# Kernel tuning notes

Measured on AMD Instinct MI355X. Metric: run time of the kernel, lower is better.

## Reference

```python
import jax, jax.numpy as jnp
import numpy as np

B, S, H = 1024, 128, 1024   # batch, seq_len, bert hidden size
E, HID, K, C = 16, 1024, 4, 3  # experts, expert hidden, top_k, num_classes
EPS = 1e-5


def _ln(x, g, b):
    mu = x.mean(-1, keepdims=True)
    var = ((x - mu) ** 2).mean(-1, keepdims=True)
    return (x - mu) / jnp.sqrt(var + EPS) * g + b


def setup_inputs() -> dict:
    key = jax.random.key(0)
    ks = jax.random.split(key, 24)
    n = lambda k, shape, s=0.02: jax.random.normal(k, shape, jnp.float32) * s
    return {
        "hidden_states": jax.random.normal(ks[0], (B, S, H), jnp.float32),
        # original BertClassificationHead
        "Wd": n(ks[1], (H, H)), "bd": jnp.zeros((H,), jnp.float32),
        "Wo": n(ks[2], (H, C)), "bo": jnp.zeros((C,), jnp.float32),
        # router
        "Wr": n(ks[3], (H, E)), "br": jnp.zeros((E,), jnp.float32),
        # stacked experts: Linear(H,HID) -> LN -> GELU -> Linear(HID,HID)
        "We1": n(ks[4], (E, H, HID)), "be1": jnp.zeros((E, HID), jnp.float32),
        "g1": jnp.ones((E, HID), jnp.float32), "beta1": jnp.zeros((E, HID), jnp.float32),
        "We2": n(ks[5], (E, HID, HID)), "be2": jnp.zeros((E, HID), jnp.float32),
        # expert_output_proj
        "Wp": n(ks[6], (HID, C)), "bp": jnp.zeros((C,), jnp.float32),
        # final_classifier: Linear(2C, C) -> LN -> ReLU -> Linear(C, C)
        "Wf1": n(ks[7], (2 * C, C)), "bf1": jnp.zeros((C,), jnp.float32),
        "gf": jnp.ones((C,), jnp.float32), "betaf": jnp.zeros((C,), jnp.float32),
        "Wf2": n(ks[8], (C, C)), "bf2": jnp.zeros((C,), jnp.float32),
    }


def reference(hidden_states, Wd, bd, Wo, bo, Wr, br, We1, be1, g1, beta1,
              We2, be2, Wp, bp, Wf1, bf1, gf, betaf, Wf2, bf2):
    cls = hidden_states[:, 0]                                   # [B,H]
    # original classifier head (dropout = identity in eval)
    original_logits = jnp.tanh(cls @ Wd + bd) @ Wo + bo         # [B,C]
    # router: top-k softmax scattered into dense [B,E] weights
    router_logits = cls @ Wr + br                               # [B,E]
    topk_vals, topk_idx = jax.lax.top_k(router_logits, K)
    topk_probs = jax.nn.softmax(topk_vals, axis=-1)
    routing_weights = jnp.zeros_like(router_logits).at[
        jnp.arange(cls.shape[0])[:, None], topk_idx].set(topk_probs)
    # experts consume mean-pooled sequence (MLPExpert mean over dim=1)
    m = hidden_states.mean(axis=1)                              # [B,H]
    h = jnp.einsum('bh,ehd->bed', m, We1) + be1                 # [B,E,HID]
    h = jax.nn.gelu(_ln(h, g1, beta1), approximate=False)
    h = jnp.einsum('bed,edf->bef', h, We2) + be2                # [B,E,HID]
    expert_logits = h @ Wp + bp                                 # [B,E,C]
    # weighted combine; routing_weights is zero for non-selected experts,
    # so this equals the sparse top-k dispatch of the original loop
    moe_output = jnp.einsum('be,bec->bc', routing_weights, expert_logits)
    combined = jnp.concatenate([original_logits, moe_output], axis=1)  # [B,2C]
    z = _ln(combined @ Wf1 + bf1, gf, betaf)
    return jax.nn.relu(z) @ Wf2 + bf2                           # [B,C]
```

## Files before the change

kernel.cpp:

```cpp
#include <hip/hip_runtime.h>
#include <math.h>

#define B_ 1024
#define S_ 128
#define H_ 1024
#define E_ 16
#define HID_ 1024
#define K_ 4
#define C_ 3
#define EPS_ 1e-5f

#define NB_CLSG 128
#define OFF_MEAN (NB_CLSG)
#define NB_MEAN 512
#define OFF_WC (OFF_MEAN + NB_MEAN)
#define NB_WC 2048
#define OFF_RT (OFF_WC + NB_WC)
#define NB_RT 128
#define OFF_BC (OFF_RT + NB_RT)
#define NB_BC 2
#define NB_P1 (OFF_BC + NB_BC)

typedef __attribute__((ext_vector_type(8))) __bf16 bf16x8;
typedef __attribute__((ext_vector_type(4))) float f32x4;
typedef __attribute__((ext_vector_type(4))) float fvec4;
typedef __attribute__((ext_vector_type(4))) unsigned short usvec4;
typedef __attribute__((ext_vector_type(8))) unsigned short usvec8;

__device__ __forceinline__ ushort bf16_rn(float f) {
  unsigned u = __float_as_uint(f);
  u += 0x7FFF + ((u >> 16) & 1);
  return (ushort)(u >> 16);
}
__device__ __forceinline__ float bf16_to_f(ushort h) {
  return __uint_as_float(((unsigned)h) << 16);
}
__device__ __forceinline__ void split2(float f, ushort& h, ushort& l) {
  h = bf16_rn(f);
  l = bf16_rn(f - bf16_to_f(h));
}
__device__ __forceinline__ void gload_lds16(const void* g, void* l) {
  __builtin_amdgcn_global_load_lds((const __attribute__((address_space(1))) void*)g,
                                   (__attribute__((address_space(3))) void*)l, 16, 0, 0);
}
#define DMA_DRAIN() do {                                  \
    asm volatile("s_waitcnt vmcnt(0)" ::: "memory");      \
    __builtin_amdgcn_sched_barrier(0);                    \
  } while (0)

__device__ __forceinline__ fvec4 nt_load4f(const float* p) {
  return __builtin_nontemporal_load((const fvec4*)p);
}
__device__ __forceinline__ void st4us(ushort* p, ushort a, ushort b, ushort c, ushort d) {
  usvec4 v; v.x = a; v.y = b; v.z = c; v.w = d;
  *(usvec4*)p = v;
}
__device__ __forceinline__ void nt_store1f(float* p, float v) {
  __builtin_nontemporal_store(v, p);
}
__device__ __forceinline__ void waveRed3(float& s0, float& s1, float& s2) {
#pragma unroll
  for (int off = 32; off; off >>= 1) {
    s0 += __shfl_down(s0, off); s1 += __shfl_down(s1, off); s2 += __shfl_down(s2, off);
  }
}

__global__ __launch_bounds__(512) void phase1_kernel(
    const float* __restrict__ hs,
    const float* __restrict__ Wd,
    const float* __restrict__ We2, const float* __restrict__ Wp, const float* __restrict__ bp,
    const float* __restrict__ Wr, const float* __restrict__ br,
    const float* __restrict__ be2,
    ushort* __restrict__ m_hi, ushort* __restrict__ m_lo,
    float* __restrict__ Wcomb, float* __restrict__ bcomb,
    int* __restrict__ topk_idx, float* __restrict__ topk_prob,
    int* __restrict__ counts, int* __restrict__ pairlist,
    float* __restrict__ tA, float* __restrict__ tB) {
  __shared__ __align__(16) ushort ldsAh0[4096], ldsAl0[4096], ldsBh0[4096], ldsBl0[4096];
  __shared__ __align__(16) ushort ldsAh1[4096], ldsAl1[4096], ldsBh1[4096], ldsBl1[4096];
  const int blk = blockIdx.x;
  const int tid = threadIdx.x;
  const int w = tid >> 6, lane = tid & 63;

  if (blk < NB_CLSG) {
    const int n0 = (blk & 7) * 128;
    const int yy = blk >> 3;
    const int mt = yy >> 1, kh = yy & 1;
    const int m0 = mt * 128;
    const int kbase = kh * 512;
    const float* sbase[2];
    size_t kstride;
    int subs0;
    if (w < 4) {
      kstride = 1;
      subs0 = w * 2;
#pragma unroll
      for (int sl = 0; sl < 2; ++sl) {
        int s = subs0 + sl;
        int b = m0 + s * 16 + (lane & 15);
        sbase[sl] = hs + (size_t)b * (S_ * H_) + ((lane >> 4) << 3);
      }
    } else {
      kstride = H_;
      subs0 = (w - 4) * 2;
#pragma unroll
      for (int sl = 0; sl < 2; ++sl) {
        int s = subs0 + sl;
        int col = n0 + s * 16 + (lane & 15);
        sbase[sl] = Wd + col + (size_t)((lane >> 4) << 3) * H_;
      }
    }
    const int wr = w >> 2, wc = w & 3;
    f32x4 acc[4][2] = {};

    auto stage = [&](int kofs, ushort* dAh, ushort* dAl, ushort* dBh, ushort* dBl) {
      ushort* dh = (w < 4) ? dAh : dBh;
      ushort* dl = (w < 4) ? dAl : dBl;
#pragma unroll
      for (int sl = 0; sl < 2; ++sl) {
        const float* p = sbase[sl] + (size_t)kofs * kstride;
        float f[8];
        if (w < 4) {
          fvec4 v0 = nt_load4f(p);
          fvec4 v1 = nt_load4f(p + 4);
          f[0] = v0.x; f[1] = v0.y; f[2] = v0.z; f[3] = v0.w;
          f[4] = v1.x; f[5] = v1.y; f[6] = v1.z; f[7] = v1.w;
        } else {
#pragma unroll
          for (int j = 0; j < 8; ++j) f[j] = p[(size_t)j * H_];
        }
        usvec8 vh, vl;
#pragma unroll
        for (int j = 0; j < 8; ++j) {
          ushort hi, lo;
          split2(f[j], hi, lo);
          vh[j] = hi; vl[j] = lo;
        }
        const int off = (subs0 + sl) * 512 + lane * 8;
        *(usvec8*)&dh[off] = vh;
        *(usvec8*)&dl[off] = vl;
      }
    };
    auto compute = [&](const ushort* Ah, const ushort* Al,
                       const ushort* Bh, const ushort* Bl) {
      bf16x8 ah[4], al[4], bh[2], bl[2];
#pragma unroll
      for (int i = 0; i < 4; ++i) {
        int off = (wr * 4 + i) * 512 + lane * 8;
        ah[i] = *(const bf16x8*)&Ah[off];
        al[i] = *(const bf16x8*)&Al[off];
      }
#pragma unroll
      for (int j = 0; j < 2; ++j) {
        int off = (wc * 2 + j) * 512 + lane * 8;
        bh[j] = *(const bf16x8*)&Bh[off];
        bl[j] = *(const bf16x8*)&Bl[off];
      }
#pragma unroll
      for (int i = 0; i < 4; ++i)
#pragma unroll
        for (int j = 0; j < 2; ++j) {
          acc[i][j] = __builtin_amdgcn_mfma_f32_16x16x32_bf16(ah[i], bh[j], acc[i][j], 0, 0, 0);
          acc[i][j] = __builtin_amdgcn_mfma_f32_16x16x32_bf16(ah[i], bl[j], acc[i][j], 0, 0, 0);
          acc[i][j] = __builtin_amdgcn_mfma_f32_16x16x32_bf16(al[i], bh[j], acc[i][j], 0, 0, 0);
        }
    };

    stage(kbase, ldsAh0, ldsAl0, ldsBh0, ldsBl0);
    DMA_DRAIN();
    __syncthreads();
#pragma unroll 1
    for (int tt = 0; tt < 8; ++tt) {
      const int t0 = tt * 2;
      stage(kbase + (t0 + 1) * 32, ldsAh1, ldsAl1, ldsBh1, ldsBl1);
      compute(ldsAh0, ldsAl0, ldsBh0, ldsBl0);
      DMA_DRAIN();
      __syncthreads();
      if (tt < 7) stage(kbase + (t0 + 2) * 32, ldsAh0, ldsAl0, ldsBh0, ldsBl0);
      compute(ldsAh1, ldsAl1, ldsBh1, ldsBl1);
      DMA_DRAIN();
      __syncthreads();
    }
    const int lr = (lane >> 4) << 2, lc = lane & 15;
    float* tp = kh ? tB : tA;
#pragma unroll
    for (int i = 0; i < 4; ++i) {
      int row = m0 + wr * 64 + i * 16 + lr;
#pragma unroll
      for (int j = 0; j < 2; ++j) {
        int col = n0 + wc * 32 + j * 16 + lc;
#pragma unroll
        for (int r = 0; r < 4; ++r)
          nt_store1f(&tp[(size_t)(row + r) * H_ + col], acc[i][j][r]);
      }
    }
  } else if (blk < OFF_WC) {
    int gid = (blk - OFF_MEAN) * 512 + tid;
    int b = gid >> 8;
    int h4 = (gid & 255) << 2;
    const float* p = hs + (size_t)b * S_ * H_ + h4;
    fvec4 v0 = nt_load4f(p);
    float sx = v0.x, sy = v0.y, sz = v0.z, sw = v0.w;
#pragma unroll 8
    for (int s = 1; s < S_; ++s) {
      fvec4 v = nt_load4f(p + (size_t)s * H_);
      sx += v.x; sy += v.y; sz += v.z; sw += v.w;
    }
    const float inv = 1.0f / (float)S_;
    float mv[4] = {sx * inv, sy * inv, sz * inv, sw * inv};
    ushort mh[4], ml[4];
#pragma unroll
    for (int i = 0; i < 4; ++i) split2(mv[i], mh[i], ml[i]);
    size_t o = (size_t)b * H_ + h4;
    st4us(&m_hi[o], mh[0], mh[1], mh[2], mh[3]);
    st4us(&m_lo[o], ml[0], ml[1], ml[2], ml[3]);
  } else if (blk < OFF_RT) {
    const int row = (blk - OFF_WC) * 8 + w;
    const float* wrp = We2 + (size_t)row * HID_;
    float s0 = 0, s1 = 0, s2 = 0;
#pragma unroll
    for (int it = 0; it < 4; ++it) {
      const int f0 = it * 256 + lane * 4;
      fvec4 v = nt_load4f(&wrp[f0]);
      s0 = fmaf(v.x, Wp[(f0 + 0) * 3 + 0], s0);
      s1 = fmaf(v.x, Wp[(f0 + 0) * 3 + 1], s1);
      s2 = fmaf(v.x, Wp[(f0 + 0) * 3 + 2], s2);
      s0 = fmaf(v.y, Wp[(f0 + 1) * 3 + 0], s0);
      s1 = fmaf(v.y, Wp[(f0 + 1) * 3 + 1], s1);
      s2 = fmaf(v.y, Wp[(f0 + 1) * 3 + 2], s2);
      s0 = fmaf(v.z, Wp[(f0 + 2) * 3 + 0], s0);
      s1 = fmaf(v.z, Wp[(f0 + 2) * 3 + 1], s1);
      s2 = fmaf(v.z, Wp[(f0 + 2) * 3 + 2], s2);
      s0 = fmaf(v.w, Wp[(f0 + 3) * 3 + 0], s0);
      s1 = fmaf(v.w, Wp[(f0 + 3) * 3 + 1], s1);
      s2 = fmaf(v.w, Wp[(f0 + 3) * 3 + 2], s2);
    }
    waveRed3(s0, s1, s2);
    if (lane == 0) {
      Wcomb[row * 3 + 0] = s0; Wcomb[row * 3 + 1] = s1; Wcomb[row * 3 + 2] = s2;
    }
  } else if (blk < OFF_BC) {
    const int b = (blk - OFF_RT) * 8 + w;
    const float* cls = hs + (size_t)b * S_ * H_;
    const int e = lane & 15, part = lane >> 4;
    float sum = 0.0f;
    for (int i = part * 256; i < part * 256 + 256; ++i)
      sum = fmaf(cls[i], Wr[i * E_ + e], sum);
    sum += __shfl_down(sum, 32);
    sum += __shfl_down(sum, 16);
    float lg[E_];
#pragma unroll
    for (int i = 0; i < E_; ++i) lg[i] = __shfl(sum, i);
    if (lane == 0) {
      for (int i = 0; i < E_; ++i) lg[i] += br[i];
      int idx[K_]; float tv[K_];
      for (int k = 0; k < K_; ++k) {
        int bi = 0; float bv = -1e30f;
        for (int i = 0; i < E_; ++i) { if (lg[i] > bv) { bv = lg[i]; bi = i; } }
        idx[k] = bi; tv[k] = bv; lg[bi] = -1e30f;
      }
      float mx = tv[0], ssum = 0.0f, p[K_];
      for (int k = 0; k < K_; ++k) { p[k] = expf(tv[k] - mx); ssum += p[k]; }
      for (int k = 0; k < K_; ++k) {
        p[k] /= ssum;
        topk_idx[b * K_ + k] = idx[k];
        topk_prob[b * K_ + k] = p[k];
        int pos = atomicAdd(&counts[idx[k]], 1);
        pairlist[idx[k] * B_ + pos] = b * K_ + k;
      }
    }
  } else {
    const int e = (blk - OFF_BC) * 8 + w;
    const float* wrp = be2 + (size_t)e * HID_;
    float s0 = 0, s1 = 0, s2 = 0;
    for (int f = lane; f < HID_; f += 64) {
      float v = wrp[f];
      s0 = fmaf(v, Wp[f * 3 + 0], s0);
      s1 = fmaf(v, Wp[f * 3 + 1], s1);
      s2 = fmaf(v, Wp[f * 3 + 2], s2);
    }
    waveRed3(s0, s1, s2);
    if (lane == 0) {
      bcomb[e * 3 + 0] = s0 + bp[0]; bcomb[e * 3 + 1] = s1 + bp[1]; bcomb[e * 3 + 2] = s2 + bp[2];
    }
  }
}

__global__ __launch_bounds__(512) void expert_gemm(
    const ushort* __restrict__ m_hi, const ushort* __restrict__ m_lo,
    const float* __restrict__ We1,
    const int* __restrict__ counts, const int* __restrict__ pairlist,
    float* __restrict__ h1A, float* __restrict__ h1B) {
  __shared__ __align__(16) ushort ldsAh0[4096], ldsAl0[4096], ldsBh0[4096], ldsBl0[4096];
  __shared__ __align__(16) ushort ldsAh1[4096], ldsAl1[4096], ldsBh1[4096], ldsBl1[4096];
  const int z = blockIdx.z;
  const int tid = threadIdx.x;
  const int lane = tid & 63, w = tid >> 6;
  const int mt = blockIdx.y >> 1, kh = blockIdx.y & 1;
  const int m0 = mt * 128, n0 = blockIdx.x * 128;
  const int kbase = kh * 512;
  const int n_e = counts[z];
  if (m0 >= n_e) return;

  const ushort* srcp[4];
  ushort* dstA0 = nullptr; ushort* dstA1 = nullptr;
  const float* bbase[2];
  int bsub[2];
  const int halfq = w & 1;
  if (w < 4) {
    const int warr = w >> 1;
    dstA0 = (warr == 0) ? ldsAh0 : ldsAl0;
    dstA1 = (warr == 0) ? ldsAh1 : ldsAl1;
    const ushort* sbase = (warr == 0) ? m_hi : m_lo;
#pragma unroll
    for (int sl = 0; sl < 4; ++sl) {
      int s = halfq * 4 + sl;
      int r = m0 + s * 16 + (lane & 15);
      if (r >= n_e) r = n_e - 1;
      r = pairlist[z * B_ + r] >> 2;
      srcp[sl] = sbase + (size_t)r * H_ + ((lane >> 4) << 3);
    }
  } else {
    const float* Wfp = We1 + (size_t)z * H_ * HID_;
#pragma unroll
    for (int sl = 0; sl < 2; ++sl) {
      int s = (w - 4) * 2 + sl;
      bsub[sl] = s;
      int col = n0 + s * 16 + (lane & 15);
      bbase[sl] = Wfp + col + (size_t)((lane >> 4) << 3) * HID_;
    }
  }

  const int wr = w >> 2, wc = w & 3;
  f32x4 acc[4][2] = {};

  auto stageA = [&](int kofs, ushort* dst) {
#pragma unroll
    for (int sl = 0; sl < 4; ++sl)
      gload_lds16(srcp[sl] + kofs, dst + (halfq * 4 + sl) * 512);
  };
  auto stageB = [&](int kofs, ushort* dBh, ushort* dBl) {
#pragma unroll
    for (int sl = 0; sl < 2; ++sl) {
      const float* bp = bbase[sl] + (size_t)kofs * HID_;
      float f[8];
#pragma unroll
      for (int j = 0; j < 8; ++j) f[j] = bp[(size_t)j * HID_];
      usvec8 vh, vl;
#pragma unroll
      for (int j = 0; j < 8; ++j) {
        ushort hi, lo;
        split2(f[j], hi, lo);
        vh[j] = hi; vl[j] = lo;
      }
      const int off = bsub[sl] * 512 + lane * 8;
      *(usvec8*)&dBh[off] = vh;
      *(usvec8*)&dBl[off] = vl;
    }
  };
  auto stage_buf0 = [&](int kofs) {
    if (w < 4) stageA(kofs, dstA0);
    else stageB(kofs, ldsBh0, ldsBl0);
  };
  auto stage_buf1 = [&](int kofs) {
    if (w < 4) stageA(kofs, dstA1);
    else stageB(kofs, ldsBh1, ldsBl1);
  };
  auto compute = [&](const ushort* Ah, const ushort* Al,
                     const ushort* Bh, const ushort* Bl) {
    bf16x8 ah[4], al[4], bh[2], bl[2];
#pragma unroll
    for (int i = 0; i < 4; ++i) {
      int off = (wr * 4 + i) * 512 + lane * 8;
      ah[i] = *(const bf16x8*)&Ah[off];
      al[i] = *(const bf16x8*)&Al[off];
    }
#pragma unroll
    for (int j = 0; j < 2; ++j) {
      int off = (wc * 2 + j) * 512 + lane * 8;
      bh[j] = *(const bf16x8*)&Bh[off];
      bl[j] = *(const bf16x8*)&Bl[off];
    }
#pragma unroll
    for (int i = 0; i < 4; ++i)
#pragma unroll
      for (int j = 0; j < 2; ++j) {
        acc[i][j] = __builtin_amdgcn_mfma_f32_16x16x32_bf16(ah[i], bh[j], acc[i][j], 0, 0, 0);
        acc[i][j] = __builtin_amdgcn_mfma_f32_16x16x32_bf16(ah[i], bl[j], acc[i][j], 0, 0, 0);
        acc[i][j] = __builtin_amdgcn_mfma_f32_16x16x32_bf16(al[i], bh[j], acc[i][j], 0, 0, 0);
      }
  };

  stage_buf0(kbase);
  DMA_DRAIN();
  __syncthreads();
#pragma unroll 1
  for (int tt = 0; tt < 8; ++tt) {
    const int t0 = tt * 2;
    stage_buf1(kbase + (t0 + 1) * 32);
    compute(ldsAh0, ldsAl0, ldsBh0, ldsBl0);
    DMA_DRAIN();
    __syncthreads();
    if (tt < 7) stage_buf0(kbase + (t0 + 2) * 32);
    compute(ldsAh1, ldsAl1, ldsBh1, ldsBl1);
    DMA_DRAIN();
    __syncthreads();
  }

  const int lr = (lane >> 4) << 2, lc = lane & 15;
  float* hp = kh ? h1B : h1A;
#pragma unroll
  for (int i = 0; i < 4; ++i) {
    int pr[4]; bool ok[4];
#pragma unroll
    for (int r = 0; r < 4; ++r) {
      int li = m0 + wr * 64 + i * 16 + lr + r;
      ok[r] = li < n_e;
      pr[r] = pairlist[z * B_ + (ok[r] ? li : n_e - 1)];
    }
#pragma unroll
    for (int j = 0; j < 2; ++j) {
      int col = n0 + wc * 32 + j * 16 + lc;
#pragma unroll
      for (int r = 0; r < 4; ++r)
        if (ok[r]) nt_store1f(&hp[(size_t)pr[r] * HID_ + col], acc[i][j][r]);
    }
  }
}

__global__ __launch_bounds__(256) void epi_kernel(
    const float* __restrict__ tA, const float* __restrict__ tB,
    const float* __restrict__ bd,
    const float* __restrict__ Wo, const float* __restrict__ bo,
    const float* __restrict__ h1A, const float* __restrict__ h1B,
    const float* __restrict__ be1,
    const float* __restrict__ g1, const float* __restrict__ beta1,
    const int* __restrict__ topk_idx, const float* __restrict__ topk_prob,
    const float* __restrict__ Wcomb, const float* __restrict__ bcomb,
    const float* __restrict__ Wf1, const float* __restrict__ bf1,
    const float* __restrict__ gf, const float* __restrict__ betaf,
    const float* __restrict__ Wf2, const float* __restrict__ bf2,
    float* __restrict__ out) {
  const int b = blockIdx.x;
  const int tid = threadIdx.x;
  const int w = tid >> 6, lane = tid & 63;
  __shared__ float sCtr[4][3];
  __shared__ float sOl[4][3];

  const int pair = b * K_ + w;
  const int e = topk_idx[pair];
  const float prob = topk_prob[pair];
  const float* hrA = h1A + (size_t)pair * HID_;
  const float* hrB = h1B + (size_t)pair * HID_;
  const float* ber = be1 + (size_t)e * HID_;
  float x[4][4];
#pragma unroll
  for (int q = 0; q < 4; ++q) {
    const int d = q * 256 + lane * 4;
    fvec4 a = nt_load4f(&hrA[d]);
    fvec4 bq = nt_load4f(&hrB[d]);
    float4 be = *(const float4*)&ber[d];
    x[q][0] = a.x + bq.x + be.x; x[q][1] = a.y + bq.y + be.y;
    x[q][2] = a.z + bq.z + be.z; x[q][3] = a.w + bq.w + be.w;
  }
  float s = 0;
#pragma unroll
  for (int q = 0; q < 4; ++q) s += x[q][0] + x[q][1] + x[q][2] + x[q][3];
#pragma unroll
  for (int off = 32; off; off >>= 1) s += __shfl_down(s, off);
  const float mu = __shfl(s, 0) * (1.0f / HID_);
  float sq = 0;
#pragma unroll
  for (int q = 0; q < 4; ++q)
#pragma unroll
    for (int i = 0; i < 4; ++i) {
      float d = x[q][i] - mu;
      sq += d * d;
    }
#pragma unroll
  for (int off = 32; off; off >>= 1) sq += __shfl_down(sq, off);
  const float inv = 1.0f / sqrtf(__shfl(sq, 0) * (1.0f / HID_) + EPS_);
  float c0 = 0, c1 = 0, c2 = 0;
#pragma unroll
  for (int q = 0; q < 4; ++q) {
    const int d = q * 256 + lane * 4;
    float4 gg = *(const float4*)&g1[(size_t)e * HID_ + d];
    float4 bb = *(const float4*)&beta1[(size_t)e * HID_ + d];
    float gv[4] = {gg.x, gg.y, gg.z, gg.w};
    float bv[4] = {bb.x, bb.y, bb.z, bb.w};
#pragma unroll
    for (int i = 0; i < 4; ++i) {
      float v = (x[q][i] - mu) * inv * gv[i] + bv[i];
      v = 0.5f * v * (1.0f + erff(v * 0.70710678118654752440f));
      const float* wc = &Wcomb[(size_t)(e * HID_ + d + i) * 3];
      c0 = fmaf(v, wc[0], c0); c1 = fmaf(v, wc[1], c1); c2 = fmaf(v, wc[2], c2);
    }
  }
  waveRed3(c0, c1, c2);
  if (lane == 0) {
    sCtr[w][0] = prob * (c0 + bcomb[e * 3 + 0]);
    sCtr[w][1] = prob * (c1 + bcomb[e * 3 + 1]);
    sCtr[w][2] = prob * (c2 + bcomb[e * 3 + 2]);
  }

  {
    const int h0 = w * 256 + lane * 4;
    fvec4 ta = nt_load4f(&tA[(size_t)b * H_ + h0]);
    fvec4 tb = nt_load4f(&tB[(size_t)b * H_ + h0]);
    float4 bdv = *(const float4*)&bd[h0];
    float tvv[4] = {tanhf(ta.x + tb.x + bdv.x), tanhf(ta.y + tb.y + bdv.y),
                    tanhf(ta.z + tb.z + bdv.z), tanhf(ta.w + tb.w + bdv.w)};
    float o0 = 0, o1 = 0, o2 = 0;
#pragma unroll
    for (int i = 0; i < 4; ++i) {
      const float* wo = &Wo[(size_t)(h0 + i) * 3];
      o0 = fmaf(tvv[i], wo[0], o0); o1 = fmaf(tvv[i], wo[1], o1); o2 = fmaf(tvv[i], wo[2], o2);
    }
    waveRed3(o0, o1, o2);
    if (lane == 0) { sOl[w][0] = o0; sOl[w][1] = o1; sOl[w][2] = o2; }
  }
  __syncthreads();

  if (tid == 0) {
    float comb[6];
#pragma unroll
    for (int c = 0; c < 3; ++c) {
      comb[c] = sOl[0][c] + sOl[1][c] + sOl[2][c] + sOl[3][c] + bo[c];
      comb[3 + c] = sCtr[0][c] + sCtr[1][c] + sCtr[2][c] + sCtr[3][c];
    }
    float z[3];
#pragma unroll
    for (int c = 0; c < 3; ++c) {
      float sv = bf1[c];
#pragma unroll
      for (int i = 0; i < 6; ++i) sv = fmaf(comb[i], Wf1[i * 3 + c], sv);
      z[c] = sv;
    }
    float mu3 = (z[0] + z[1] + z[2]) * (1.0f / 3.0f);
    float v0 = z[0] - mu3, v1 = z[1] - mu3, v2 = z[2] - mu3;
    float var = (v0 * v0 + v1 * v1 + v2 * v2) * (1.0f / 3.0f);
    float inv3 = 1.0f / sqrtf(var + EPS_);
    float r[3];
#pragma unroll
    for (int c = 0; c < 3; ++c) {
      float zz = (z[c] - mu3) * inv3 * gf[c] + betaf[c];
      r[c] = zz > 0.0f ? zz : 0.0f;
    }
#pragma unroll
    for (int c = 0; c < 3; ++c) {
      float sv = bf2[c];
#pragma unroll
      for (int i = 0; i < 3; ++i) sv = fmaf(r[i], Wf2[i * 3 + c], sv);
      out[b * 3 + c] = sv;
    }
  }
}

extern "C" void kernel_launch(void* const* d_in, const int* in_sizes, int n_in,
                              void* d_out, int out_size, void* d_ws, size_t ws_size,
                              hipStream_t stream) {
  const float* hs    = (const float*)d_in[0];
  const float* Wd    = (const float*)d_in[1];
  const float* bd    = (const float*)d_in[2];
  const float* Wo    = (const float*)d_in[3];
  const float* bo    = (const float*)d_in[4];
  const float* Wr    = (const float*)d_in[5];
  const float* br    = (const float*)d_in[6];
  const float* We1   = (const float*)d_in[7];
  const float* be1   = (const float*)d_in[8];
  const float* g1    = (const float*)d_in[9];
  const float* beta1 = (const float*)d_in[10];
  const float* We2   = (const float*)d_in[11];
  const float* be2   = (const float*)d_in[12];
  const float* Wp    = (const float*)d_in[13];
  const float* bp    = (const float*)d_in[14];
  const float* Wf1   = (const float*)d_in[15];
  const float* bf1   = (const float*)d_in[16];
  const float* gf    = (const float*)d_in[17];
  const float* betaf = (const float*)d_in[18];
  const float* Wf2   = (const float*)d_in[19];
  const float* bf2   = (const float*)d_in[20];
  float* out = (float*)d_out;

  char* w = (char*)d_ws;
  size_t off = 0;
  auto alloc = [&](size_t bytes) {
    void* p = w + off;
    off = (off + bytes + 255) & ~(size_t)255;
    return p;
  };
  ushort* m_hi   = (ushort*)alloc((size_t)B_ * H_ * 2);
  ushort* m_lo   = (ushort*)alloc((size_t)B_ * H_ * 2);
  float* ws_tA   = (float*)alloc((size_t)B_ * H_ * 4);
  float* ws_tB   = (float*)alloc((size_t)B_ * H_ * 4);
  float* ws_h1A  = (float*)alloc((size_t)B_ * K_ * HID_ * 4);
  float* ws_h1B  = (float*)alloc((size_t)B_ * K_ * HID_ * 4);
  float* ws_wc   = (float*)alloc((size_t)E_ * HID_ * 3 * 4);
  float* ws_bc   = (float*)alloc(E_ * 3 * 4);
  float* ws_prob = (float*)alloc(B_ * K_ * 4);
  int* ws_idx = (int*)alloc(B_ * K_ * 4);
  int* ws_cnt = (int*)alloc(E_ * 4);
  int* ws_pl  = (int*)alloc(E_ * B_ * 4);
  if (off > ws_size) return;

  hipMemsetAsync(ws_cnt, 0, E_ * sizeof(int), stream);

  phase1_kernel<<<NB_P1, 512, 0, stream>>>(hs, Wd, We2, Wp, bp, Wr, br, be2,
                                           m_hi, m_lo, ws_wc, ws_bc,
                                           ws_idx, ws_prob, ws_cnt, ws_pl,
                                           ws_tA, ws_tB);
  expert_gemm<<<dim3(8, 16, 16), 512, 0, stream>>>(m_hi, m_lo, We1, ws_cnt, ws_pl,
                                                   ws_h1A, ws_h1B);
  epi_kernel<<<B_, 256, 0, stream>>>(ws_tA, ws_tB, bd, Wo, bo, ws_h1A, ws_h1B, be1,
                                     g1, beta1, ws_idx, ws_prob, ws_wc, ws_bc,
                                     Wf1, bf1, gf, betaf, Wf2, bf2, out);
}
```

Baseline: 235.2 us.

## Double M tile per block in expert GEMM to reuse converted B tiles

Each expert_gemm block now covers 256 pair rows instead of 128, staging two A tiles per K step against one shared B tile. The fp32 We1 loads and their split into hi/lo bf16 are done once per 256 rows instead of once per 128 rows. This halves the grid's M dimension and cuts redundant weight traffic and conversion. In exchange it doubles accumulator registers and raises LDS use to 96 KB per block, which may lower occupancy. Load imbalance also grows when experts hold few rows.

```diff
diff --git a/kernel.cpp b/kernel.cpp
--- a/kernel.cpp
+++ b/kernel.cpp
@@ -291,34 +291,35 @@
     const float* __restrict__ We1,
     const int* __restrict__ counts, const int* __restrict__ pairlist,
     float* __restrict__ h1A, float* __restrict__ h1B) {
-  __shared__ __align__(16) ushort ldsAh0[4096], ldsAl0[4096], ldsBh0[4096], ldsBl0[4096];
-  __shared__ __align__(16) ushort ldsAh1[4096], ldsAl1[4096], ldsBh1[4096], ldsBl1[4096];
+  __shared__ __align__(16) ushort A0h0[4096], A0l0[4096], A0h1[4096], A0l1[4096];
+  __shared__ __align__(16) ushort A1h0[4096], A1l0[4096], A1h1[4096], A1l1[4096];
+  __shared__ __align__(16) ushort B0h[4096], B0l[4096], B1h[4096], B1l[4096];
   const int z = blockIdx.z;
   const int tid = threadIdx.x;
   const int lane = tid & 63, w = tid >> 6;
-  const int mt = blockIdx.y >> 1, kh = blockIdx.y & 1;
-  const int m0 = mt * 128, n0 = blockIdx.x * 128;
+  const int mtp = blockIdx.y >> 1, kh = blockIdx.y & 1;
+  const int m0base = mtp * 256;
+  const int n0 = blockIdx.x * 128;
   const int kbase = kh * 512;
   const int n_e = counts[z];
-  if (m0 >= n_e) return;
-
-  const ushort* srcp[4];
+  if (m0base >= n_e) return;
+
+  const ushort* srcp[8];
   ushort* dstA0 = nullptr; ushort* dstA1 = nullptr;
   const float* bbase[2];
   int bsub[2];
-  const int halfq = w & 1;
   if (w < 4) {
-    const int warr = w >> 1;
-    dstA0 = (warr == 0) ? ldsAh0 : ldsAl0;
-    dstA1 = (warr == 0) ? ldsAh1 : ldsAl1;
-    const ushort* sbase = (warr == 0) ? m_hi : m_lo;
-#pragma unroll
-    for (int sl = 0; sl < 4; ++sl) {
-      int s = halfq * 4 + sl;
-      int r = m0 + s * 16 + (lane & 15);
+    const int amt = w >> 1;
+    const int ahl = w & 1;
+    dstA0 = (w == 0) ? A0h0 : (w == 1) ? A0l0 : (w == 2) ? A0h1 : A0l1;
+    dstA1 = (w == 0) ? A1h0 : (w == 1) ? A1l0 : (w == 2) ? A1h1 : A1l1;
+    const ushort* sbase = (ahl == 0) ? m_hi : m_lo;
+#pragma unroll
+    for (int s = 0; s < 8; ++s) {
+      int r = m0base + amt * 128 + s * 16 + (lane & 15);
       if (r >= n_e) r = n_e - 1;
       r = pairlist[z * B_ + r] >> 2;
-      srcp[sl] = sbase + (size_t)r * H_ + ((lane >> 4) << 3);
+      srcp[s] = sbase + (size_t)r * H_ + ((lane >> 4) << 3);
     }
   } else {
     const float* Wfp = We1 + (size_t)z * H_ * HID_;
@@ -332,12 +333,13 @@
   }
 
   const int wr = w >> 2, wc = w & 3;
-  f32x4 acc[4][2] = {};
+  f32x4 acc0[4][2] = {};
+  f32x4 acc1[4][2] = {};
 
   auto stageA = [&](int kofs, ushort* dst) {
 #pragma unroll
-    for (int sl = 0; sl < 4; ++sl)
-      gload_lds16(srcp[sl] + kofs, dst + (halfq * 4 + sl) * 512);
+    for (int s = 0; s < 8; ++s)
+      gload_lds16(srcp[s] + kofs, dst + s * 512);
   };
   auto stageB = [&](int kofs, ushort* dBh, ushort* dBl) {
 #pragma unroll
@@ -360,35 +362,56 @@
   };
   auto stage_buf0 = [&](int kofs) {
     if (w < 4) stageA(kofs, dstA0);
-    else stageB(kofs, ldsBh0, ldsBl0);
+    else stageB(kofs, B0h, B0l);
   };
   auto stage_buf1 = [&](int kofs) {
     if (w < 4) stageA(kofs, dstA1);
-    else stageB(kofs, ldsBh1, ldsBl1);
+    else stageB(kofs, B1h, B1l);
   };
-  auto compute = [&](const ushort* Ah, const ushort* Al,
+  auto compute = [&](const ushort* Ah0, const ushort* Al0,
+                     const ushort* Ah1, const ushort* Al1,
                      const ushort* Bh, const ushort* Bl) {
-    bf16x8 ah[4], al[4], bh[2], bl[2];
-#pragma unroll
-    for (int i = 0; i < 4; ++i) {
-      int off = (wr * 4 + i) * 512 + lane * 8;
-      ah[i] = *(const bf16x8*)&Ah[off];
-      al[i] = *(const bf16x8*)&Al[off];
-    }
+    bf16x8 bh[2], bl[2];
 #pragma unroll
     for (int j = 0; j < 2; ++j) {
       int off = (wc * 2 + j) * 512 + lane * 8;
       bh[j] = *(const bf16x8*)&Bh[off];
       bl[j] = *(const bf16x8*)&Bl[off];
     }
-#pragma unroll
-    for (int i = 0; i < 4; ++i)
-#pragma unroll
-      for (int j = 0; j < 2; ++j) {
-        acc[i][j] = __builtin_amdgcn_mfma_f32_16x16x32_bf16(ah[i], bh[j], acc[i][j], 0, 0, 0);
-        acc[i][j] = __builtin_amdgcn_mfma_f32_16x16x32_bf16(ah[i], bl[j], acc[i][j], 0, 0, 0);
-        acc[i][j] = __builtin_amdgcn_mfma_f32_16x16x32_bf16(al[i], bh[j], acc[i][j], 0, 0, 0);
-      }
+    {
+      bf16x8 ah[4], al[4];
+#pragma unroll
+      for (int i = 0; i < 4; ++i) {
+        int off = (wr * 4 + i) * 512 + lane * 8;
+        ah[i] = *(const bf16x8*)&Ah0[off];
+        al[i] = *(const bf16x8*)&Al0[off];
+      }
+#pragma unroll
+      for (int i = 0; i < 4; ++i)
+#pragma unroll
+        for (int j = 0; j < 2; ++j) {
+          acc0[i][j] = __builtin_amdgcn_mfma_f32_16x16x32_bf16(ah[i], bh[j], acc0[i][j], 0, 0, 0);
+          acc0[i][j] = __builtin_amdgcn_mfma_f32_16x16x32_bf16(ah[i], bl[j], acc0[i][j], 0, 0, 0);
+          acc0[i][j] = __builtin_amdgcn_mfma_f32_16x16x32_bf16(al[i], bh[j], acc0[i][j], 0, 0, 0);
+        }
+    }
+    {
+      bf16x8 ah[4], al[4];
+#pragma unroll
+      for (int i = 0; i < 4; ++i) {
+        int off = (wr * 4 + i) * 512 + lane * 8;
+        ah[i] = *(const bf16x8*)&Ah1[off];
+        al[i] = *(const bf16x8*)&Al1[off];
+      }
+#pragma unroll
+      for (int i = 0; i < 4; ++i)
+#pragma unroll
+        for (int j = 0; j < 2; ++j) {
+          acc1[i][j] = __builtin_amdgcn_mfma_f32_16x16x32_bf16(ah[i], bh[j], acc1[i][j], 0, 0, 0);
+          acc1[i][j] = __builtin_amdgcn_mfma_f32_16x16x32_bf16(ah[i], bl[j], acc1[i][j], 0, 0, 0);
+          acc1[i][j] = __builtin_amdgcn_mfma_f32_16x16x32_bf16(al[i], bh[j], acc1[i][j], 0, 0, 0);
+        }
+    }
   };
 
   stage_buf0(kbase);
@@ -398,11 +421,11 @@
   for (int tt = 0; tt < 8; ++tt) {
     const int t0 = tt * 2;
     stage_buf1(kbase + (t0 + 1) * 32);
-    compute(ldsAh0, ldsAl0, ldsBh0, ldsBl0);
+    compute(A0h0, A0l0, A0h1, A0l1, B0h, B0l);
     DMA_DRAIN();
     __syncthreads();
     if (tt < 7) stage_buf0(kbase + (t0 + 2) * 32);
-    compute(ldsAh1, ldsAl1, ldsBh1, ldsBl1);
+    compute(A1h0, A1l0, A1h1, A1l1, B1h, B1l);
     DMA_DRAIN();
     __syncthreads();
   }
@@ -410,20 +433,25 @@
   const int lr = (lane >> 4) << 2, lc = lane & 15;
   float* hp = kh ? h1B : h1A;
 #pragma unroll
-  for (int i = 0; i < 4; ++i) {
-    int pr[4]; bool ok[4];
-#pragma unroll
-    for (int r = 0; r < 4; ++r) {
-      int li = m0 + wr * 64 + i * 16 + lr + r;
-      ok[r] = li < n_e;
-      pr[r] = pairlist[z * B_ + (ok[r] ? li : n_e - 1)];
-    }
-#pragma unroll
-    for (int j = 0; j < 2; ++j) {
-      int col = n0 + wc * 32 + j * 16 + lc;
-#pragma unroll
-      for (int r = 0; r < 4; ++r)
-        if (ok[r]) nt_store1f(&hp[(size_t)pr[r] * HID_ + col], acc[i][j][r]);
+  for (int mt = 0; mt < 2; ++mt) {
+#pragma unroll
+    for (int i = 0; i < 4; ++i) {
+      int pr[4]; bool ok[4];
+#pragma unroll
+      for (int r = 0; r < 4; ++r) {
+        int li = m0base + mt * 128 + wr * 64 + i * 16 + lr + r;
+        ok[r] = li < n_e;
+        pr[r] = pairlist[z * B_ + (ok[r] ? li : n_e - 1)];
+      }
+#pragma unroll
+      for (int j = 0; j < 2; ++j) {
+        int col = n0 + wc * 32 + j * 16 + lc;
+#pragma unroll
+        for (int r = 0; r < 4; ++r) {
+          float v = mt ? acc1[i][j][r] : acc0[i][j][r];
+          if (ok[r]) nt_store1f(&hp[(size_t)pr[r] * HID_ + col], v);
+        }
+      }
     }
   }
 }
@@ -609,8 +637,8 @@
                                            m_hi, m_lo, ws_wc, ws_bc,
                                            ws_idx, ws_prob, ws_cnt, ws_pl,
                                            ws_tA, ws_tB);
-  expert_gemm<<<dim3(8, 16, 16), 512, 0, stream>>>(m_hi, m_lo, We1, ws_cnt, ws_pl,
-                                                   ws_h1A, ws_h1B);
+  expert_gemm<<<dim3(8, 8, 16), 512, 0, stream>>>(m_hi, m_lo, We1, ws_cnt, ws_pl,
+                                                  ws_h1A, ws_h1B);
   epi_kernel<<<B_, 256, 0, stream>>>(ws_tA, ws_tB, bd, Wo, bo, ws_h1A, ws_h1B, be1,
                                      g1, beta1, ws_idx, ws_prob, ws_wc, ws_bc,
                                      Wf1, bf1, gf, betaf, Wf2, bf2, out);
```

Result: slower. 256.9 us (+9.2%).

## Move CLS dense GEMM into expert GEMM launch, slim prep kernel to 256 threads

Applied to the files above, without the earlier changes.

The CLS @ Wd GEMM blocks move out of the first-phase kernel into the expert GEMM grid as an extra z-slice (z==16). The prep kernel then holds only the mean, Wcomb, router and bias-combine work at 256 threads with no large LDS arrays. The aim is to give the light prep kernel better occupancy and to let the dense GEMM run alongside the sparse expert GEMM, filling idle CUs left by early-exit expert blocks. The dense GEMM now waits on prep to finish, which adds it to the critical path after the mean reduction.

```diff
diff --git a/kernel.cpp b/kernel.cpp
--- a/kernel.cpp
+++ b/kernel.cpp
@@ -10,16 +10,14 @@
 #define C_ 3
 #define EPS_ 1e-5f
 
-#define NB_CLSG 128
-#define OFF_MEAN (NB_CLSG)
-#define NB_MEAN 512
-#define OFF_WC (OFF_MEAN + NB_MEAN)
-#define NB_WC 2048
+#define NB_MEAN 1024
+#define NB_WC 4096
+#define NB_RT 256
+#define NB_BC 4
+#define OFF_WC (NB_MEAN)
 #define OFF_RT (OFF_WC + NB_WC)
-#define NB_RT 128
 #define OFF_BC (OFF_RT + NB_RT)
-#define NB_BC 2
-#define NB_P1 (OFF_BC + NB_BC)
+#define NB_PREP (OFF_BC + NB_BC)
 
 typedef __attribute__((ext_vector_type(8))) __bf16 bf16x8;
 typedef __attribute__((ext_vector_type(4))) float f32x4;
@@ -65,137 +63,20 @@
   }
 }
 
-__global__ __launch_bounds__(512) void phase1_kernel(
+__global__ __launch_bounds__(256) void prep_kernel(
     const float* __restrict__ hs,
-    const float* __restrict__ Wd,
     const float* __restrict__ We2, const float* __restrict__ Wp, const float* __restrict__ bp,
     const float* __restrict__ Wr, const float* __restrict__ br,
     const float* __restrict__ be2,
     ushort* __restrict__ m_hi, ushort* __restrict__ m_lo,
     float* __restrict__ Wcomb, float* __restrict__ bcomb,
     int* __restrict__ topk_idx, float* __restrict__ topk_prob,
-    int* __restrict__ counts, int* __restrict__ pairlist,
-    float* __restrict__ tA, float* __restrict__ tB) {
-  __shared__ __align__(16) ushort ldsAh0[4096], ldsAl0[4096], ldsBh0[4096], ldsBl0[4096];
-  __shared__ __align__(16) ushort ldsAh1[4096], ldsAl1[4096], ldsBh1[4096], ldsBl1[4096];
+    int* __restrict__ counts, int* __restrict__ pairlist) {
   const int blk = blockIdx.x;
   const int tid = threadIdx.x;
-  const int w = tid >> 6, lane = tid & 63;
-
-  if (blk < NB_CLSG) {
-    const int n0 = (blk & 7) * 128;
-    const int yy = blk >> 3;
-    const int mt = yy >> 1, kh = yy & 1;
-    const int m0 = mt * 128;
-    const int kbase = kh * 512;
-    const float* sbase[2];
-    size_t kstride;
-    int subs0;
-    if (w < 4) {
-      kstride = 1;
-      subs0 = w * 2;
-#pragma unroll
-      for (int sl = 0; sl < 2; ++sl) {
-        int s = subs0 + sl;
-        int b = m0 + s * 16 + (lane & 15);
-        sbase[sl] = hs + (size_t)b * (S_ * H_) + ((lane >> 4) << 3);
-      }
-    } else {
-      kstride = H_;
-      subs0 = (w - 4) * 2;
-#pragma unroll
-      for (int sl = 0; sl < 2; ++sl) {
-        int s = subs0 + sl;
-        int col = n0 + s * 16 + (lane & 15);
-        sbase[sl] = Wd + col + (size_t)((lane >> 4) << 3) * H_;
-      }
-    }
-    const int wr = w >> 2, wc = w & 3;
-    f32x4 acc[4][2] = {};
-
-    auto stage = [&](int kofs, ushort* dAh, ushort* dAl, ushort* dBh, ushort* dBl) {
-      ushort* dh = (w < 4) ? dAh : dBh;
-      ushort* dl = (w < 4) ? dAl : dBl;
-#pragma unroll
-      for (int sl = 0; sl < 2; ++sl) {
-        const float* p = sbase[sl] + (size_t)kofs * kstride;
-        float f[8];
-        if (w < 4) {
-          fvec4 v0 = nt_load4f(p);
-          fvec4 v1 = nt_load4f(p + 4);
-          f[0] = v0.x; f[1] = v0.y; f[2] = v0.z; f[3] = v0.w;
-          f[4] = v1.x; f[5] = v1.y; f[6] = v1.z; f[7] = v1.w;
-        } else {
-#pragma unroll
-          for (int j = 0; j < 8; ++j) f[j] = p[(size_t)j * H_];
-        }
-        usvec8 vh, vl;
-#pragma unroll
-        for (int j = 0; j < 8; ++j) {
-          ushort hi, lo;
-          split2(f[j], hi, lo);
-          vh[j] = hi; vl[j] = lo;
-        }
-        const int off = (subs0 + sl) * 512 + lane * 8;
-        *(usvec8*)&dh[off] = vh;
-        *(usvec8*)&dl[off] = vl;
-      }
-    };
-    auto compute = [&](const ushort* Ah, const ushort* Al,
-                       const ushort* Bh, const ushort* Bl) {
-      bf16x8 ah[4], al[4], bh[2], bl[2];
-#pragma unroll
-      for (int i = 0; i < 4; ++i) {
-        int off = (wr * 4 + i) * 512 + lane * 8;
-        ah[i] = *(const bf16x8*)&Ah[off];
-        al[i] = *(const bf16x8*)&Al[off];
-      }
-#pragma unroll
-      for (int j = 0; j < 2; ++j) {
-        int off = (wc * 2 + j) * 512 + lane * 8;
-        bh[j] = *(const bf16x8*)&Bh[off];
-        bl[j] = *(const bf16x8*)&Bl[off];
-      }
-#pragma unroll
-      for (int i = 0; i < 4; ++i)
-#pragma unroll
-        for (int j = 0; j < 2; ++j) {
-          acc[i][j] = __builtin_amdgcn_mfma_f32_16x16x32_bf16(ah[i], bh[j], acc[i][j], 0, 0, 0);
-          acc[i][j] = __builtin_amdgcn_mfma_f32_16x16x32_bf16(ah[i], bl[j], acc[i][j], 0, 0, 0);
-          acc[i][j] = __builtin_amdgcn_mfma_f32_16x16x32_bf16(al[i], bh[j], acc[i][j], 0, 0, 0);
-        }
-    };
-
-    stage(kbase, ldsAh0, ldsAl0, ldsBh0, ldsBl0);
-    DMA_DRAIN();
-    __syncthreads();
-#pragma unroll 1
-    for (int tt = 0; tt < 8; ++tt) {
-      const int t0 = tt * 2;
-      stage(kbase + (t0 + 1) * 32, ldsAh1, ldsAl1, ldsBh1, ldsBl1);
-      compute(ldsAh0, ldsAl0, ldsBh0, ldsBl0);
-      DMA_DRAIN();
-      __syncthreads();
-      if (tt < 7) stage(kbase + (t0 + 2) * 32, ldsAh0, ldsAl0, ldsBh0, ldsBl0);
-      compute(ldsAh1, ldsAl1, ldsBh1, ldsBl1);
-      DMA_DRAIN();
-      __syncthreads();
-    }
-    const int lr = (lane >> 4) << 2, lc = lane & 15;
-    float* tp = kh ? tB : tA;
-#pragma unroll
-    for (int i = 0; i < 4; ++i) {
-      int row = m0 + wr * 64 + i * 16 + lr;
-#pragma unroll
-      for (int j = 0; j < 2; ++j) {
-        int col = n0 + wc * 32 + j * 16 + lc;
-#pragma unroll
-        for (int r = 0; r < 4; ++r)
-          nt_store1f(&tp[(size_t)(row + r) * H_ + col], acc[i][j][r]);
-      }
-    }
-  } else if (blk < OFF_WC) {
-    int gid = (blk - OFF_MEAN) * 512 + tid;
+
+  if (blk < NB_MEAN) {
+    int gid = blk * 256 + tid;
     int b = gid >> 8;
     int h4 = (gid & 255) << 2;
     const float* p = hs + (size_t)b * S_ * H_ + h4;
@@ -215,7 +96,8 @@
     st4us(&m_hi[o], mh[0], mh[1], mh[2], mh[3]);
     st4us(&m_lo[o], ml[0], ml[1], ml[2], ml[3]);
   } else if (blk < OFF_RT) {
-    const int row = (blk - OFF_WC) * 8 + w;
+    const int row = (blk - OFF_WC) * 4 + (tid >> 6);
+    const int lane = tid & 63;
     const float* wrp = We2 + (size_t)row * HID_;
     float s0 = 0, s1 = 0, s2 = 0;
 #pragma unroll
@@ -240,7 +122,8 @@
       Wcomb[row * 3 + 0] = s0; Wcomb[row * 3 + 1] = s1; Wcomb[row * 3 + 2] = s2;
     }
   } else if (blk < OFF_BC) {
-    const int b = (blk - OFF_RT) * 8 + w;
+    const int lane = tid & 63;
+    const int b = (blk - OFF_RT) * 4 + (tid >> 6);
     const float* cls = hs + (size_t)b * S_ * H_;
     const int e = lane & 15, part = lane >> 4;
     float sum = 0.0f;
@@ -270,7 +153,8 @@
       }
     }
   } else {
-    const int e = (blk - OFF_BC) * 8 + w;
+    const int e = (blk - OFF_BC) * 4 + (tid >> 6);
+    const int lane = tid & 63;
     const float* wrp = be2 + (size_t)e * HID_;
     float s0 = 0, s1 = 0, s2 = 0;
     for (int f = lane; f < HID_; f += 64) {
@@ -286,10 +170,12 @@
   }
 }
 
-__global__ __launch_bounds__(512) void expert_gemm(
+__global__ __launch_bounds__(512) void gemm_mega(
+    const float* __restrict__ hs,
     const ushort* __restrict__ m_hi, const ushort* __restrict__ m_lo,
-    const float* __restrict__ We1,
+    const float* __restrict__ Wd, const float* __restrict__ We1,
     const int* __restrict__ counts, const int* __restrict__ pairlist,
+    float* __restrict__ tA, float* __restrict__ tB,
     float* __restrict__ h1A, float* __restrict__ h1B) {
   __shared__ __align__(16) ushort ldsAh0[4096], ldsAl0[4096], ldsBh0[4096], ldsBl0[4096];
   __shared__ __align__(16) ushort ldsAh1[4096], ldsAl1[4096], ldsBh1[4096], ldsBl1[4096];
@@ -299,6 +185,117 @@
   const int mt = blockIdx.y >> 1, kh = blockIdx.y & 1;
   const int m0 = mt * 128, n0 = blockIdx.x * 128;
   const int kbase = kh * 512;
+  const int wr = w >> 2, wc = w & 3;
+  const int lr = (lane >> 4) << 2, lc = lane & 15;
+
+  if (z == 16) {
+    const float* sbase[2];
+    size_t kstride;
+    int subs0;
+    if (w < 4) {
+      kstride = 1;
+      subs0 = w * 2;
+#pragma unroll
+      for (int sl = 0; sl < 2; ++sl) {
+        int s = subs0 + sl;
+        int b = m0 + s * 16 + (lane & 15);
+        sbase[sl] = hs + (size_t)b * (S_ * H_) + ((lane >> 4) << 3);
+      }
+    } else {
+      kstride = H_;
+      subs0 = (w - 4) * 2;
+#pragma unroll
+      for (int sl = 0; sl < 2; ++sl) {
+        int s = subs0 + sl;
+        int col = n0 + s * 16 + (lane & 15);
+        sbase[sl] = Wd + col + (size_t)((lane >> 4) << 3) * H_;
+      }
+    }
+    f32x4 acc[4][2] = {};
+
+    auto stage = [&](int kofs, ushort* dAh, ushort* dAl, ushort* dBh, ushort* dBl) {
+      ushort* dh = (w < 4) ? dAh : dBh;
+      ushort* dl = (w < 4) ? dAl : dBl;
+#pragma unroll
+      for (int sl = 0; sl < 2; ++sl) {
+        const float* p = sbase[sl] + (size_t)kofs * kstride;
+        float f[8];
+        if (w < 4) {
+          fvec4 v0 = nt_load4f(p);
+          fvec4 v1 = nt_load4f(p + 4);
+          f[0] = v0.x; f[1] = v0.y; f[2] = v0.z; f[3] = v0.w;
+          f[4] = v1.x; f[5] = v1.y; f[6] = v1.z; f[7] = v1.w;
+        } else {
+#pragma unroll
+          for (int j = 0; j < 8; ++j) f[j] = p[(size_t)j * H_];
+        }
+        usvec8 vh, vl;
+#pragma unroll
+        for (int j = 0; j < 8; ++j) {
+          ushort hi, lo;
+          split2(f[j], hi, lo);
+          vh[j] = hi; vl[j] = lo;
+        }
+        const int off = (subs0 + sl) * 512 + lane * 8;
+        *(usvec8*)&dh[off] = vh;
+        *(usvec8*)&dl[off] = vl;
+      }
+    };
+    auto compute = [&](const ushort* Ah, const ushort* Al,
+                       const ushort* Bh, const ushort* Bl) {
+      bf16x8 ah[4], al[4], bh[2], bl[2];
+#pragma unroll
+      for (int i = 0; i < 4; ++i) {
+        int off = (wr * 4 + i) * 512 + lane * 8;
+        ah[i] = *(const bf16x8*)&Ah[off];
+        al[i] = *(const bf16x8*)&Al[off];
+      }
+#pragma unroll
+      for (int j = 0; j < 2; ++j) {
+        int off = (wc * 2 + j) * 512 + lane * 8;
+        bh[j] = *(const bf16x8*)&Bh[off];
+        bl[j] = *(const bf16x8*)&Bl[off];
+      }
+#pragma unroll
+      for (int i = 0; i < 4; ++i)
+#pragma unroll
+        for (int j = 0; j < 2; ++j) {
+          acc[i][j] = __builtin_amdgcn_mfma_f32_16x16x32_bf16(ah[i], bh[j], acc[i][j], 0, 0, 0);
+          acc[i][j] = __builtin_amdgcn_mfma_f32_16x16x32_bf16(ah[i], bl[j], acc[i][j], 0, 0, 0);
+          acc[i][j] = __builtin_amdgcn_mfma_f32_16x16x32_bf16(al[i], bh[j], acc[i][j], 0, 0, 0);
+        }
+    };
+
+    stage(kbase, ldsAh0, ldsAl0, ldsBh0, ldsBl0);
+    DMA_DRAIN();
+    __syncthreads();
+#pragma unroll 1
+    for (int tt = 0; tt < 8; ++tt) {
+      const int t0 = tt * 2;
+      stage(kbase + (t0 + 1) * 32, ldsAh1, ldsAl1, ldsBh1, ldsBl1);
+      compute(ldsAh0, ldsAl0, ldsBh0, ldsBl0);
+      DMA_DRAIN();
+      __syncthreads();
+      if (tt < 7) stage(kbase + (t0 + 2) * 32, ldsAh0, ldsAl0, ldsBh0, ldsBl0);
+      compute(ldsAh1, ldsAl1, ldsBh1, ldsBl1);
+      DMA_DRAIN();
+      __syncthreads();
+    }
+    float* tp = kh ? tB : tA;
+#pragma unroll
+    for (int i = 0; i < 4; ++i) {
+      int row = m0 + wr * 64 + i * 16 + lr;
+#pragma unroll
+      for (int j = 0; j < 2; ++j) {
+        int col = n0 + wc * 32 + j * 16 + lc;
+#pragma unroll
+        for (int r = 0; r < 4; ++r)
+          nt_store1f(&tp[(size_t)(row + r) * H_ + col], acc[i][j][r]);
+      }
+    }
+    return;
+  }
+
   const int n_e = counts[z];
   if (m0 >= n_e) return;
 
@@ -331,7 +328,6 @@
     }
   }
 
-  const int wr = w >> 2, wc = w & 3;
   f32x4 acc[4][2] = {};
 
   auto stageA = [&](int kofs, ushort* dst) {
@@ -407,7 +403,6 @@
     __syncthreads();
   }
 
-  const int lr = (lane >> 4) << 2, lc = lane & 15;
   float* hp = kh ? h1B : h1A;
 #pragma unroll
   for (int i = 0; i < 4; ++i) {
@@ -605,12 +600,12 @@
 
   hipMemsetAsync(ws_cnt, 0, E_ * sizeof(int), stream);
 
-  phase1_kernel<<<NB_P1, 512, 0, stream>>>(hs, Wd, We2, Wp, bp, Wr, br, be2,
+  prep_kernel<<<NB_PREP, 256, 0, stream>>>(hs, We2, Wp, bp, Wr, br, be2,
                                            m_hi, m_lo, ws_wc, ws_bc,
-                                           ws_idx, ws_prob, ws_cnt, ws_pl,
-                                           ws_tA, ws_tB);
-  expert_gemm<<<dim3(8, 16, 16), 512, 0, stream>>>(m_hi, m_lo, We1, ws_cnt, ws_pl,
-                                                   ws_h1A, ws_h1B);
+                                           ws_idx, ws_prob, ws_cnt, ws_pl);
+  gemm_mega<<<dim3(8, 16, 17), 512, 0, stream>>>(hs, m_hi, m_lo, Wd, We1,
+                                                 ws_cnt, ws_pl,
+                                                 ws_tA, ws_tB, ws_h1A, ws_h1B);
   epi_kernel<<<B_, 256, 0, stream>>>(ws_tA, ws_tB, bd, Wo, bo, ws_h1A, ws_h1B, be1,
                                      g1, beta1, ws_idx, ws_prob, ws_wc, ws_bc,
                                      Wf1, bf1, gf, betaf, Wf2, bf2, out);
```

Measured after the change: 252.9 us. 1.08x slower.
